# Kernel optimization log

Measured on AMD Instinct MI355X. Metric: run time of the kernel, lower is better.

The kernel has to match this reference:

```python
import jax, jax.numpy as jnp
import numpy as np

NUM_HEADS = 16


def dct_matrix(n, dtype=jnp.float32):
    # Orthonormal DCT-II matrix, matching the torch double-loop construction.
    i = jnp.arange(n, dtype=dtype)[:, None]
    j = jnp.arange(n, dtype=dtype)[None, :]
    m = jnp.sqrt(2.0 / n) * jnp.cos(jnp.pi * i * (2.0 * j + 1.0) / (2.0 * n))
    m = m.at[0, :].set(jnp.sqrt(1.0 / n))
    return m


def setup_inputs() -> dict:
    key = jax.random.key(0)
    ks = jax.random.split(key, 7)
    B, N, C = 8, 1024, 1024
    n_tasks, n_frq = 10, 3000
    return {
        "x": jax.random.normal(ks[0], (B, N, C), jnp.float32),
        "W_qkv": jax.random.normal(ks[1], (3 * C, C), jnp.float32) * 0.02,
        "W_proj": jax.random.normal(ks[2], (C, C), jnp.float32) * 0.02,
        "b_proj": jnp.zeros((C,), jnp.float32),
        "coef_k": jax.random.normal(ks[3], (n_tasks, n_frq), jnp.float32),
        "coef_v": jax.random.normal(ks[4], (n_tasks, n_frq), jnp.float32),
        "indices": jax.random.randint(ks[5], (n_tasks, n_frq), 0, C * C, jnp.int32),
        "task": 4,
    }


def _dct_lora_weight(coef, idx, Bm, d, dtype):
    # Scatter per-task frequency coefficients into the d x d DCT plane and sum
    # across tasks (sum commutes with the linear inverse transform), then
    # inverse 2D DCT: W = Bm^T @ S @ Bm.
    S = jnp.zeros((d * d,), dtype).at[idx.reshape(-1)].add(coef.reshape(-1))
    return Bm.T @ S.reshape(d, d) @ Bm


def reference(x, W_qkv, W_proj, b_proj, coef_k, coef_v, indices, task):
    B, N, C = x.shape
    H = NUM_HEADS
    hd = C // H
    scale = hd ** (-0.5)

    qkv = (x @ W_qkv.T).reshape(B, N, 3, H, hd).transpose(2, 0, 3, 1, 4)
    q, k, v = qkv[0], qkv[1], qkv[2]  # each (B, H, N, hd)

    T = task + 1  # tasks 0..task participate
    Bm = dct_matrix(C, x.dtype)
    Wk = _dct_lora_weight(coef_k[:T], indices[:T], Bm, C, x.dtype)
    Wv = _dct_lora_weight(coef_v[:T], indices[:T], Bm, C, x.dtype)

    # F.linear(x, W) == x @ W.T ; reshape to heads as in torch code
    k = k + (x @ Wk.T).reshape(B, N, H, hd).transpose(0, 2, 1, 3)
    v = v + (x @ Wv.T).reshape(B, N, H, hd).transpose(0, 2, 1, 3)

    attn = jax.nn.softmax(jnp.einsum("bhnd,bhmd->bhnm", q, k) * scale, axis=-1)
    out = jnp.einsum("bhnm,bhmd->bhnd", attn, v)
    out = out.transpose(0, 2, 1, 3).reshape(B, N, C)
    return out @ W_proj.T + b_proj
```

## Files before the change

### kernel.cpp

```cpp
#include <hip/hip_runtime.h>
#include <math.h>

#define NFRQ 3000

typedef __bf16 bf16;
typedef __attribute__((ext_vector_type(8))) __bf16 bf16x8;
typedef __attribute__((ext_vector_type(4))) __bf16 bf16x4;
typedef __attribute__((ext_vector_type(4))) float floatx4;

__device__ __forceinline__ floatx4 mfma16(bf16x8 a, bf16x8 b, floatx4 c) {
  return __builtin_amdgcn_mfma_f32_16x16x32_bf16(a, b, c, 0, 0, 0);
}

__device__ __forceinline__ void async_load16(const bf16* g, bf16* l) {
  __builtin_amdgcn_global_load_lds(
      (const __attribute__((address_space(1))) unsigned int*)g,
      (__attribute__((address_space(3))) unsigned int*)l, 16, 0, 0);
}

__device__ __forceinline__ float fexp2(float x) {
  return __builtin_amdgcn_exp2f(x);
}

__global__ __launch_bounds__(256) void prep_kernel(
    const float* __restrict__ W_qkv, const float* __restrict__ W_proj,
    const float* __restrict__ x, const float* __restrict__ Sf,
    bf16* __restrict__ Bmtb, bf16* __restrict__ Wcbq,
    bf16* __restrict__ Wprojb, bf16* __restrict__ xb,
    bf16* __restrict__ S2b) {
  int r = blockIdx.x;
  if (r < 1024) {
    int base = r * 1024 + (int)threadIdx.x * 4;
    const float cst = 0.04419417382415922f;
    const float w = 1.5339807878856412e-3f;
    bf16x4 o;
#pragma unroll
    for (int u = 0; u < 4; ++u) {
      int t = base + u;
      int j = t >> 10, i = t & 1023;
      int K = (i * (2 * j + 1)) & 4095;
      float v = (i == 0) ? 0.03125f : cst * __cosf((float)K * w);
      o[u] = (__bf16)v;
    }
    *(bf16x4*)&Bmtb[base] = o;
    return;
  }
  const float* src;
  bf16* dst;
  float scale = 1.0f;
  int i;
  if (r < 2048) {
    i = (r - 1024) * 256 + threadIdx.x;
    src = W_qkv; dst = Wcbq;
    scale = 0.18033688011112042f;
  } else if (r < 3072) {
    i = (r - 2048) * 256 + threadIdx.x;
    src = W_proj; dst = Wprojb;
  } else if (r < 11264) {
    i = (r - 3072) * 256 + threadIdx.x;
    src = x; dst = xb;
  } else {
    i = (r - 11264) * 256 + threadIdx.x;
    src = Sf; dst = S2b;
  }
  float4 f = ((const float4*)src)[i];
  bf16x4 o = {(__bf16)(f.x * scale), (__bf16)(f.y * scale),
              (__bf16)(f.z * scale), (__bf16)(f.w * scale)};
  *(bf16x4*)&dst[(size_t)i * 4] = o;
}

__global__ __launch_bounds__(256) void scatter_s(const float* __restrict__ coef_k,
                                                 const float* __restrict__ coef_v,
                                                 const int* __restrict__ idx,
                                                 const int* __restrict__ task,
                                                 float* __restrict__ S) {
  int nz = blockIdx.x * 256 + threadIdx.x;
  if (nz >= 10 * NFRQ || nz >= (*task + 1) * NFRQ) return;
  int id = idx[nz];
  atomicAdd(S + id, coef_k[nz]);
  atomicAdd(S + (1u << 20) + id, coef_v[nz]);
}

__global__ __launch_bounds__(512, 2) void gemm256_qkv(const bf16* __restrict__ A,
                                                      const bf16* __restrict__ B,
                                                      bf16* __restrict__ Cb,
                                                      bf16* __restrict__ vt) {
  __shared__ bf16 As[2][256][64];
  __shared__ bf16 Bs[2][256][64];
  int t = threadIdx.x, w = t >> 6, lane = t & 63;
  int q15 = lane & 15, quad = lane >> 4;
  int lid = blockIdx.x + gridDim.x * blockIdx.y;
  int band = gridDim.y >> 3;
  int xcd = lid & 7, tt = lid >> 3;
  int by = xcd * band + tt % band;
  int bx = tt / band;
  int m0 = by * 256, n0 = bx * 256;
  int wm = (w >> 2) * 128, wn = (w & 3) * 64;

  floatx4 acc[8][4];
#pragma unroll
  for (int i = 0; i < 8; ++i)
#pragma unroll
    for (int j = 0; j < 4; ++j) acc[i][j] = (floatx4){0.f, 0.f, 0.f, 0.f};

  int sr = lane >> 3, sc = lane & 7;
  const bf16* Agl = A + (size_t)(m0 + sr) * 1024 + (sc ^ sr) * 8;
  const bf16* Bgl = B + (size_t)(n0 + sr) * 1024 + (sc ^ sr) * 8;

#pragma unroll
  for (int s = 0; s < 4; ++s) {
    int rb = w * 32 + s * 8;
    async_load16(Agl + (size_t)rb * 1024, &As[0][rb][0]);
    async_load16(Bgl + (size_t)rb * 1024, &Bs[0][rb][0]);
  }

  for (int kt = 0; kt < 16; ++kt) {
    int cur = kt & 1;
    if (kt + 1 < 16) {
      int k0 = (kt + 1) * 64;
#pragma unroll
      for (int s = 0; s < 4; ++s) {
        int rb = w * 32 + s * 8;
        async_load16(Agl + (size_t)rb * 1024 + k0, &As[cur ^ 1][rb][0]);
        async_load16(Bgl + (size_t)rb * 1024 + k0, &Bs[cur ^ 1][rb][0]);
      }
      asm volatile("s_waitcnt vmcnt(8)\n\ts_barrier" ::: "memory");
    } else {
      asm volatile("s_waitcnt vmcnt(0)\n\ts_barrier" ::: "memory");
    }
    int rp = q15 & 7;
#pragma unroll
    for (int kk = 0; kk < 2; ++kk) {
      int kc = kk * 4 + quad;
      int ksw = (kc ^ rp) * 8;
      bf16x8 af[8], bfr[4];
#pragma unroll
      for (int i = 0; i < 8; ++i)
        af[i] = *(const bf16x8*)&As[cur][wm + i * 16 + q15][ksw];
#pragma unroll
      for (int j = 0; j < 4; ++j)
        bfr[j] = *(const bf16x8*)&Bs[cur][wn + j * 16 + q15][ksw];
#pragma unroll
      for (int i = 0; i < 8; ++i)
#pragma unroll
        for (int j = 0; j < 4; ++j)
          acc[i][j] = mfma16(af[i], bfr[j], acc[i][j]);
    }
    asm volatile("s_waitcnt lgkmcnt(0)\n\ts_barrier" ::: "memory");
  }

  if (n0 >= 2048) {
#pragma unroll
    for (int i = 0; i < 8; ++i) {
      int gm = m0 + wm + i * 16 + quad * 4;
      int p = gm >> 10, mi = gm & 1023;
#pragma unroll
      for (int j = 0; j < 4; ++j) {
        int vchan = (n0 + wn - 2048) + j * 16 + q15;
        bf16x4 pk = {(__bf16)acc[i][j][0], (__bf16)acc[i][j][1],
                     (__bf16)acc[i][j][2], (__bf16)acc[i][j][3]};
        *(bf16x4*)&vt[((((size_t)p << 10) | vchan) << 10) | mi] = pk;
      }
    }
    return;
  }

#pragma unroll
  for (int i = 0; i < 8; ++i)
#pragma unroll
    for (int r = 0; r < 4; ++r) {
      int gm = m0 + wm + i * 16 + quad * 4 + r;
      size_t rowo = (size_t)gm * 3072 + n0 + wn;
#pragma unroll
      for (int j = 0; j < 4; ++j) {
        int col = j * 16 + q15;
        Cb[rowo + col] = (__bf16)acc[i][j][r];
      }
    }
}

__global__ __launch_bounds__(256) void gemm64_bf16_nt(const bf16* __restrict__ A,
                                                      const bf16* __restrict__ B,
                                                      bf16* __restrict__ Cb,
                                                      float* __restrict__ Cf,
                                                      const float* __restrict__ addend,
                                                      const float* __restrict__ bias,
                                                      bf16* __restrict__ vt,
                                                      int vt_col0,
                                                      int N) {
  __shared__ bf16 As[2][4][64][8];
  __shared__ bf16 Bs[2][4][64][8];
  size_t zoff = (size_t)blockIdx.z << 20;
  B += zoff;
  if (Cb) Cb += zoff;
  if (addend) addend += zoff;
  int t = threadIdx.x, w = t >> 6, lane = t & 63;
  int q15 = lane & 15, quad = lane >> 4;
  int lid = blockIdx.x + gridDim.x * blockIdx.y;
  int band = gridDim.y >> 3;
  int xcd = lid & 7, tt = lid >> 3;
  int by = xcd * band + tt % band;
  int bx = tt / band;
  int m0 = by * 64, n0 = bx * 64;
  int wm = (w >> 1) * 32, wn = (w & 1) * 32;
  floatx4 acc[2][2];
#pragma unroll
  for (int i = 0; i < 2; ++i)
#pragma unroll
    for (int j = 0; j < 2; ++j) acc[i][j] = (floatx4){0.f, 0.f, 0.f, 0.f};

  const bf16* Ag = A + (size_t)(m0 + lane) * 1024 + w * 8;
  const bf16* Bg = B + (size_t)(n0 + lane) * 1024 + w * 8;

  async_load16(Ag, &As[0][w][0][0]);
  async_load16(Bg, &Bs[0][w][0][0]);

  for (int it = 0; it < 32; ++it) {
    int cur = it & 1;
    __syncthreads();
    if (it + 1 < 32) {
      int k0 = (it + 1) * 32;
      async_load16(Ag + k0, &As[cur ^ 1][w][0][0]);
      async_load16(Bg + k0, &Bs[cur ^ 1][w][0][0]);
    }
    bf16x8 af[2], bfr[2];
#pragma unroll
    for (int i = 0; i < 2; ++i)
      af[i] = *(const bf16x8*)&As[cur][quad][wm + i * 16 + q15][0];
#pragma unroll
    for (int j = 0; j < 2; ++j)
      bfr[j] = *(const bf16x8*)&Bs[cur][quad][wn + j * 16 + q15][0];
#pragma unroll
    for (int i = 0; i < 2; ++i)
#pragma unroll
      for (int j = 0; j < 2; ++j) acc[i][j] = mfma16(af[i], bfr[j], acc[i][j]);
  }

  if (vt && (n0 + wn) >= vt_col0) {
#pragma unroll
    for (int i = 0; i < 2; ++i) {
      int gm = m0 + wm + i * 16 + quad * 4;
      int p = gm >> 10, mi = gm & 1023;
#pragma unroll
      for (int j = 0; j < 2; ++j) {
        int vchan = (n0 + wn - vt_col0) + j * 16 + q15;
        bf16x4 pk = {(__bf16)acc[i][j][0], (__bf16)acc[i][j][1],
                     (__bf16)acc[i][j][2], (__bf16)acc[i][j][3]};
        *(bf16x4*)&vt[((((size_t)p << 10) | vchan) << 10) | mi] = pk;
      }
    }
    return;
  }

#pragma unroll
  for (int i = 0; i < 2; ++i)
#pragma unroll
    for (int r = 0; r < 4; ++r) {
      int gm = m0 + wm + i * 16 + quad * 4 + r;
      size_t rowo = (size_t)gm * N + n0 + wn;
#pragma unroll
      for (int j = 0; j < 2; ++j) {
        int col = j * 16 + q15;
        float v = acc[i][j][r];
        if (Cf) {
          Cf[rowo + col] = v + (bias ? bias[n0 + wn + col] : 0.f);
        } else {
          if (addend) v += addend[rowo + col];
          Cb[rowo + col] = (__bf16)v;
        }
      }
    }
}

__global__ __launch_bounds__(256) void attn_mfma(const bf16* __restrict__ qkvb,
                                                 const bf16* __restrict__ Vt,
                                                 bf16* __restrict__ attn_out) {
  __shared__ __align__(16) char smem[49152];
  bf16 (*Qs)[128][8] = (bf16(*)[128][8])smem;
  bf16* PsB = (bf16*)smem;
  bf16 (*Ks)[8][64][8] = (bf16(*)[8][64][8])(smem + 16384);
  bf16 (*Vs)[8][64][8] = (bf16(*)[8][64][8])(smem + 32768);

  int t = threadIdx.x, w = t >> 6, lane = t & 63;
  int q15 = lane & 15, quad = lane >> 4;
  int lid = blockIdx.x + (blockIdx.y << 3);
  int xcd = lid & 7, rr = lid >> 3;
  int q0 = (rr & 7) * 128;
  int bh = xcd + ((rr >> 3) << 3);
  int b = bh >> 4, h = bh & 15;

  const bf16* Qg = qkvb + (size_t)(b * 1024 + q0) * 3072 + h * 64;
  const bf16* Kg = qkvb + (size_t)(b * 1024) * 3072 + 1024 + h * 64;
  const bf16* Vg = Vt + (size_t)(bh * 64) * 1024;

#pragma unroll
  for (int cc = 0; cc < 2; ++cc) {
    int kc = w * 2 + cc;
    async_load16(Qg + (size_t)lane * 3072 + kc * 8,        &Qs[kc][0][0]);
    async_load16(Qg + (size_t)(64 + lane) * 3072 + kc * 8, &Qs[kc][64][0]);
  }
  {
    const bf16* Kg2 = Kg + (size_t)lane * 3072;
    const bf16* Vg2 = Vg + (size_t)lane * 1024;
    async_load16(Kg2 + (w * 2) * 8,     &Ks[0][w * 2][0][0]);
    async_load16(Kg2 + (w * 2 + 1) * 8, &Ks[0][w * 2 + 1][0][0]);
    async_load16(Vg2 + (w * 2) * 8,     &Vs[0][w * 2][0][0]);
    async_load16(Vg2 + (w * 2 + 1) * 8, &Vs[0][w * 2 + 1][0][0]);
  }
  __syncthreads();

  bf16x8 qfr[2][2];
#pragma unroll
  for (int ks = 0; ks < 2; ++ks)
#pragma unroll
    for (int nt = 0; nt < 2; ++nt)
      qfr[ks][nt] = *(const bf16x8*)&Qs[ks * 4 + quad][w * 32 + nt * 16 + q15][0];

  floatx4 oacc[4][2];
  float l_i[2] = {0.f, 0.f};
#pragma unroll
  for (int nt = 0; nt < 2; ++nt)
#pragma unroll
    for (int mt = 0; mt < 4; ++mt) oacc[mt][nt] = (floatx4){0.f, 0.f, 0.f, 0.f};

  for (int kt = 0; kt < 16; ++kt) {
    int cur = kt & 1;
    __syncthreads();
    if (kt + 1 < 16) {
      int kv0n = (kt + 1) * 64;
      const bf16* Kg3 = Kg + (size_t)(kv0n + lane) * 3072;
      const bf16* Vg3 = Vg + (size_t)lane * 1024 + kv0n;
      async_load16(Kg3 + (w * 2) * 8,     &Ks[cur ^ 1][w * 2][0][0]);
      async_load16(Kg3 + (w * 2 + 1) * 8, &Ks[cur ^ 1][w * 2 + 1][0][0]);
      async_load16(Vg3 + (w * 2) * 8,     &Vs[cur ^ 1][w * 2][0][0]);
      async_load16(Vg3 + (w * 2 + 1) * 8, &Vs[cur ^ 1][w * 2 + 1][0][0]);
    }

    floatx4 sacc[4][2];
#pragma unroll
    for (int mt = 0; mt < 4; ++mt)
#pragma unroll
      for (int nt = 0; nt < 2; ++nt) sacc[mt][nt] = (floatx4){0.f, 0.f, 0.f, 0.f};
#pragma unroll
    for (int ks = 0; ks < 2; ++ks) {
      bf16x8 kf[4];
#pragma unroll
      for (int mt = 0; mt < 4; ++mt)
        kf[mt] = *(const bf16x8*)&Ks[cur][ks * 4 + quad][mt * 16 + q15][0];
#pragma unroll
      for (int mt = 0; mt < 4; ++mt)
#pragma unroll
        for (int nt = 0; nt < 2; ++nt)
          sacc[mt][nt] = mfma16(kf[mt], qfr[ks][nt], sacc[mt][nt]);
    }

#pragma unroll
    for (int nt = 0; nt < 2; ++nt) {
      float rsum = 0.f;
#pragma unroll
      for (int mt = 0; mt < 4; ++mt)
#pragma unroll
        for (int r = 0; r < 4; ++r) {
          float p = fexp2(sacc[mt][nt][r]);
          sacc[mt][nt][r] = p;
          rsum += p;
        }
      rsum += __shfl_xor(rsum, 16);
      rsum += __shfl_xor(rsum, 32);
      l_i[nt] += rsum;
    }

#pragma unroll
    for (int nt = 0; nt < 2; ++nt)
#pragma unroll
      for (int mt = 0; mt < 4; ++mt) {
        bf16x4 pk = {(__bf16)sacc[mt][nt][0], (__bf16)sacc[mt][nt][1],
                     (__bf16)sacc[mt][nt][2], (__bf16)sacc[mt][nt][3]};
        int kc = mt * 2 + (quad >> 1);
        *(bf16x4*)&PsB[(size_t)(w * 2 + nt) * 1024 + kc * 128 + q15 * 8 + (quad & 1) * 4] = pk;
      }

#pragma unroll
    for (int ks = 0; ks < 2; ++ks) {
      bf16x8 vf[4], pf[2];
#pragma unroll
      for (int mt = 0; mt < 4; ++mt)
        vf[mt] = *(const bf16x8*)&Vs[cur][ks * 4 + quad][mt * 16 + q15][0];
#pragma unroll
      for (int nt = 0; nt < 2; ++nt)
        pf[nt] = *(const bf16x8*)&PsB[(size_t)(w * 2 + nt) * 1024 + (ks * 4 + quad) * 128 + q15 * 8];
#pragma unroll
      for (int mt = 0; mt < 4; ++mt)
#pragma unroll
        for (int nt = 0; nt < 2; ++nt) oacc[mt][nt] = mfma16(vf[mt], pf[nt], oacc[mt][nt]);
    }
  }

  __syncthreads();
  bf16* T = (bf16*)smem + w * 2304;
#pragma unroll
  for (int nt = 0; nt < 2; ++nt) {
    float inv = 1.f / l_i[nt];
#pragma unroll
    for (int mt = 0; mt < 4; ++mt) {
      bf16x4 pk = {(__bf16)(oacc[mt][nt][0] * inv), (__bf16)(oacc[mt][nt][1] * inv),
                   (__bf16)(oacc[mt][nt][2] * inv), (__bf16)(oacc[mt][nt][3] * inv)};
      *(bf16x4*)&T[(nt * 16 + q15) * 72 + mt * 16 + quad * 4] = pk;
    }
  }
  __syncthreads();
  int row = lane >> 1, ch = (lane & 1) * 32;
  const bf16* Tr = T + row * 72 + ch;
  bf16* outp = attn_out + (size_t)(b * 1024 + q0 + w * 32 + row) * 1024 + h * 64 + ch;
#pragma unroll
  for (int i = 0; i < 4; ++i) *(bf16x8*)&outp[i * 8] = *(const bf16x8*)&Tr[i * 8];
}

extern "C" void kernel_launch(void* const* d_in, const int* in_sizes, int n_in,
                              void* d_out, int out_size, void* d_ws, size_t ws_size,
                              hipStream_t stream) {
  (void)in_sizes; (void)n_in; (void)out_size; (void)ws_size;
  const float* x       = (const float*)d_in[0];
  const float* W_qkv   = (const float*)d_in[1];
  const float* W_proj  = (const float*)d_in[2];
  const float* b_proj  = (const float*)d_in[3];
  const float* coef_k  = (const float*)d_in[4];
  const float* coef_v  = (const float*)d_in[5];
  const int*   indices = (const int*)d_in[6];
  const int*   task    = (const int*)d_in[7];

  char* w8 = (char*)d_ws;
  float* Sf     = (float*)(w8);
  bf16*  S2b    = (bf16*) (w8 + (8u  << 20));
  bf16*  Tt     = (bf16*) (w8 + (12u << 20));
  bf16*  Bmtb   = (bf16*) (w8 + (16u << 20));
  bf16*  Wcb    = (bf16*) (w8 + (18u << 20));
  bf16*  xb     = (bf16*) (w8 + (24u << 20));
  bf16*  qkvb   = (bf16*) (w8 + (40u << 20));
  bf16*  Vt     = (bf16*) (w8 + (88u << 20));
  bf16*  Wprojb = (bf16*) (w8 + (104u << 20));
  bf16*  attnout= (bf16*) (w8);

  hipMemsetAsync(Sf, 0, (size_t)8 << 20, stream);
  scatter_s<<<118, 256, 0, stream>>>(coef_k, coef_v, indices, task, Sf);
  prep_kernel<<<13312, 256, 0, stream>>>(W_qkv, W_proj, x, Sf,
                                         Bmtb, Wcb, Wprojb, xb, S2b);

  gemm64_bf16_nt<<<dim3(16, 32), 256, 0, stream>>>(S2b, Bmtb, nullptr, nullptr,
                                                   nullptr, nullptr, Tt, 0, 1024);
  gemm64_bf16_nt<<<dim3(16, 16, 2), 256, 0, stream>>>(Bmtb, Tt, Wcb + (1u << 20), nullptr,
                                                      W_qkv + (1u << 20), nullptr, nullptr,
                                                      1 << 30, 1024);

  gemm256_qkv<<<dim3(12, 32), 512, 0, stream>>>(xb, Wcb, qkvb, Vt);

  attn_mfma<<<dim3(8, 128), 256, 0, stream>>>(qkvb, Vt, attnout);

  gemm64_bf16_nt<<<dim3(16, 128), 256, 0, stream>>>(attnout, Wprojb, nullptr, (float*)d_out,
                                                    nullptr, b_proj, nullptr, 1 << 30, 1024);
}
```

Before: 344.9 us.

## Use 256x128 tiled GEMM for projection and single-buffer V in attention

Replaces the 64-wide projection GEMM with a new 512-thread 256x128 tile kernel that uses swizzled LDS layout, double-buffered async loads and XCD-aware block mapping, to raise data reuse per tile. In attention, the V tile drops from double to single buffering, which shrinks LDS to allow more resident blocks. The next V tile is loaded after the PV MFMAs with explicit waitcnt/barrier control. This adds extra barriers and puts V load latency on the critical path between iterations.

```diff
diff --git a/kernel.cpp b/kernel.cpp
--- a/kernel.cpp
+++ b/kernel.cpp
@@ -175,6 +175,90 @@
       for (int j = 0; j < 4; ++j) {
         int col = j * 16 + q15;
         Cb[rowo + col] = (__bf16)acc[i][j][r];
+      }
+    }
+}
+
+__global__ __launch_bounds__(512) void gemm256_proj(const bf16* __restrict__ A,
+                                                    const bf16* __restrict__ B,
+                                                    float* __restrict__ Cf,
+                                                    const float* __restrict__ bias) {
+  __shared__ bf16 As[2][256][64];
+  __shared__ bf16 Bs[2][128][64];
+  int t = threadIdx.x, w = t >> 6, lane = t & 63;
+  int q15 = lane & 15, quad = lane >> 4;
+  int lid = blockIdx.x + gridDim.x * blockIdx.y;
+  int band = gridDim.y >> 3;
+  int xcd = lid & 7, tt = lid >> 3;
+  int by = xcd * band + tt % band;
+  int bx = tt / band;
+  int m0 = by * 256, n0 = bx * 128;
+  int wm = (w >> 2) * 128, wn = (w & 3) * 32;
+
+  floatx4 acc[8][2];
+#pragma unroll
+  for (int i = 0; i < 8; ++i)
+#pragma unroll
+    for (int j = 0; j < 2; ++j) acc[i][j] = (floatx4){0.f, 0.f, 0.f, 0.f};
+
+  int sr = lane >> 3, sc = lane & 7;
+  const bf16* Agl = A + (size_t)(m0 + sr) * 1024 + (sc ^ sr) * 8;
+  const bf16* Bgl = B + (size_t)(n0 + sr) * 1024 + (sc ^ sr) * 8;
+
+#pragma unroll
+  for (int s = 0; s < 4; ++s)
+    async_load16(Agl + (size_t)(w * 32 + s * 8) * 1024, &As[0][w * 32 + s * 8][0]);
+#pragma unroll
+  for (int s = 0; s < 2; ++s)
+    async_load16(Bgl + (size_t)(w * 16 + s * 8) * 1024, &Bs[0][w * 16 + s * 8][0]);
+
+  for (int kt = 0; kt < 16; ++kt) {
+    int cur = kt & 1;
+    if (kt + 1 < 16) {
+      int k0 = (kt + 1) * 64;
+#pragma unroll
+      for (int s = 0; s < 4; ++s)
+        async_load16(Agl + (size_t)(w * 32 + s * 8) * 1024 + k0,
+                     &As[cur ^ 1][w * 32 + s * 8][0]);
+#pragma unroll
+      for (int s = 0; s < 2; ++s)
+        async_load16(Bgl + (size_t)(w * 16 + s * 8) * 1024 + k0,
+                     &Bs[cur ^ 1][w * 16 + s * 8][0]);
+      asm volatile("s_waitcnt vmcnt(6)\n\ts_barrier" ::: "memory");
+    } else {
+      asm volatile("s_waitcnt vmcnt(0)\n\ts_barrier" ::: "memory");
+    }
+    int rp = q15 & 7;
+#pragma unroll
+    for (int kk = 0; kk < 2; ++kk) {
+      int kc = kk * 4 + quad;
+      int ksw = (kc ^ rp) * 8;
+      bf16x8 af[8], bfr[2];
+#pragma unroll
+      for (int i = 0; i < 8; ++i)
+        af[i] = *(const bf16x8*)&As[cur][wm + i * 16 + q15][ksw];
+#pragma unroll
+      for (int j = 0; j < 2; ++j)
+        bfr[j] = *(const bf16x8*)&Bs[cur][wn + j * 16 + q15][ksw];
+#pragma unroll
+      for (int i = 0; i < 8; ++i)
+#pragma unroll
+        for (int j = 0; j < 2; ++j)
+          acc[i][j] = mfma16(af[i], bfr[j], acc[i][j]);
+    }
+    asm volatile("s_waitcnt lgkmcnt(0)\n\ts_barrier" ::: "memory");
+  }
+
+#pragma unroll
+  for (int i = 0; i < 8; ++i)
+#pragma unroll
+    for (int r = 0; r < 4; ++r) {
+      int gm = m0 + wm + i * 16 + quad * 4 + r;
+      size_t rowo = (size_t)gm * 1024 + n0 + wn;
+#pragma unroll
+      for (int j = 0; j < 2; ++j) {
+        int col = j * 16 + q15;
+        Cf[rowo + col] = acc[i][j][r] + bias[n0 + wn + col];
       }
     }
 }
@@ -275,11 +359,11 @@
 __global__ __launch_bounds__(256) void attn_mfma(const bf16* __restrict__ qkvb,
                                                  const bf16* __restrict__ Vt,
                                                  bf16* __restrict__ attn_out) {
-  __shared__ __align__(16) char smem[49152];
+  __shared__ __align__(16) char smem[40960];
   bf16 (*Qs)[128][8] = (bf16(*)[128][8])smem;
   bf16* PsB = (bf16*)smem;
   bf16 (*Ks)[8][64][8] = (bf16(*)[8][64][8])(smem + 16384);
-  bf16 (*Vs)[8][64][8] = (bf16(*)[8][64][8])(smem + 32768);
+  bf16 (*Vs)[64][8] = (bf16(*)[64][8])(smem + 32768);
 
   int t = threadIdx.x, w = t >> 6, lane = t & 63;
   int q15 = lane & 15, quad = lane >> 4;
@@ -304,8 +388,8 @@
     const bf16* Vg2 = Vg + (size_t)lane * 1024;
     async_load16(Kg2 + (w * 2) * 8,     &Ks[0][w * 2][0][0]);
     async_load16(Kg2 + (w * 2 + 1) * 8, &Ks[0][w * 2 + 1][0][0]);
-    async_load16(Vg2 + (w * 2) * 8,     &Vs[0][w * 2][0][0]);
-    async_load16(Vg2 + (w * 2 + 1) * 8, &Vs[0][w * 2 + 1][0][0]);
+    async_load16(Vg2 + (w * 2) * 8,     &Vs[w * 2][0][0]);
+    async_load16(Vg2 + (w * 2 + 1) * 8, &Vs[w * 2 + 1][0][0]);
   }
   __syncthreads();
 
@@ -325,15 +409,12 @@
 
   for (int kt = 0; kt < 16; ++kt) {
     int cur = kt & 1;
-    __syncthreads();
+    asm volatile("s_waitcnt vmcnt(2) lgkmcnt(0)\n\ts_barrier" ::: "memory");
     if (kt + 1 < 16) {
       int kv0n = (kt + 1) * 64;
       const bf16* Kg3 = Kg + (size_t)(kv0n + lane) * 3072;
-      const bf16* Vg3 = Vg + (size_t)lane * 1024 + kv0n;
       async_load16(Kg3 + (w * 2) * 8,     &Ks[cur ^ 1][w * 2][0][0]);
       async_load16(Kg3 + (w * 2 + 1) * 8, &Ks[cur ^ 1][w * 2 + 1][0][0]);
-      async_load16(Vg3 + (w * 2) * 8,     &Vs[cur ^ 1][w * 2][0][0]);
-      async_load16(Vg3 + (w * 2 + 1) * 8, &Vs[cur ^ 1][w * 2 + 1][0][0]);
     }
 
     floatx4 sacc[4][2];
@@ -380,12 +461,17 @@
         *(bf16x4*)&PsB[(size_t)(w * 2 + nt) * 1024 + kc * 128 + q15 * 8 + (quad & 1) * 4] = pk;
       }
 
+    if (kt + 1 < 16)
+      asm volatile("s_waitcnt vmcnt(2)\n\ts_barrier" ::: "memory");
+    else
+      asm volatile("s_waitcnt vmcnt(0)\n\ts_barrier" ::: "memory");
+
 #pragma unroll
     for (int ks = 0; ks < 2; ++ks) {
       bf16x8 vf[4], pf[2];
 #pragma unroll
       for (int mt = 0; mt < 4; ++mt)
-        vf[mt] = *(const bf16x8*)&Vs[cur][ks * 4 + quad][mt * 16 + q15][0];
+        vf[mt] = *(const bf16x8*)&Vs[ks * 4 + quad][mt * 16 + q15][0];
 #pragma unroll
       for (int nt = 0; nt < 2; ++nt)
         pf[nt] = *(const bf16x8*)&PsB[(size_t)(w * 2 + nt) * 1024 + (ks * 4 + quad) * 128 + q15 * 8];
@@ -393,6 +479,14 @@
       for (int mt = 0; mt < 4; ++mt)
 #pragma unroll
         for (int nt = 0; nt < 2; ++nt) oacc[mt][nt] = mfma16(vf[mt], pf[nt], oacc[mt][nt]);
+    }
+
+    if (kt + 1 < 16) {
+      asm volatile("s_waitcnt lgkmcnt(0)\n\ts_barrier" ::: "memory");
+      int kv0n = (kt + 1) * 64;
+      const bf16* Vg3 = Vg + (size_t)lane * 1024 + kv0n;
+      async_load16(Vg3 + (w * 2) * 8,     &Vs[w * 2][0][0]);
+      async_load16(Vg3 + (w * 2 + 1) * 8, &Vs[w * 2 + 1][0][0]);
     }
   }
 
@@ -456,6 +550,5 @@
 
   attn_mfma<<<dim3(8, 128), 256, 0, stream>>>(qkvb, Vt, attnout);
 
-  gemm64_bf16_nt<<<dim3(16, 128), 256, 0, stream>>>(attnout, Wprojb, nullptr, (float*)d_out,
-                                                    nullptr, b_proj, nullptr, 1 << 30, 1024);
-}
+  gemm256_proj<<<dim3(8, 32), 512, 0, stream>>>(attnout, Wprojb, (float*)d_out, b_proj);
+}
```

Measured after the change: 304.3 us. 1.13x faster.
